# Performance work log

Hardware: AMD Instinct MI355X
Metric: run time of the kernel (lower is better)

The kernel has to match this reference:

```python
import jax, jax.numpy as jnp
import numpy as np
from jax import lax


def _normalizer(x):
    # faithful to: x / norm(x, axis=-1, keepdims=True) + 1e-10
    return x / jnp.linalg.norm(x, axis=-1, keepdims=True) + 1e-10


def setup_inputs() -> dict:
    key = jax.random.key(0)
    k1, k2, k3, k4 = jax.random.split(key, 4)
    Q, D, N, C = 4096, 768, 100000, 1000
    return {
        "feature": jax.random.normal(k1, (Q, D), dtype=jnp.float32),
        "logit": jax.random.normal(k2, (Q, C), dtype=jnp.float32),
        "bank_feas": jax.random.normal(k3, (N, D), dtype=jnp.float32),
        "bank_logits": jax.random.normal(k4, (N, C), dtype=jnp.float32),
        "K": 100,
    }


def reference(feature, logit, bank_feas, bank_logits, K):
    # --- setup(): build bank_guide ---
    bank_confs = jax.nn.logsumexp(bank_logits, axis=-1)          # [N]
    bank_guide = _normalizer(bank_feas) * bank_confs[:, None]    # [N, D]

    # --- forward() ---
    feas_norm = _normalizer(feature)                             # [Q, D]
    energy = jax.nn.logsumexp(logit, axis=-1)                    # [Q]

    # exact kNN inner-product search (faiss IndexFlatIP) = GEMM + top-k
    sims = jnp.einsum("qd,nd->qn", feas_norm, bank_guide)        # [Q, N]
    topk_vals, _ = lax.top_k(sims, K)                            # [Q, K]
    conf = jnp.mean(topk_vals, axis=-1)                          # [Q]

    score = conf * energy
    return -score
```

## Files before the change

kernel.cpp:

```cpp
#include <hip/hip_runtime.h>
#include <hip/hip_bf16.h>

#define QROWS 4096
#define DDIM  768
#define NBANK 100000
#define CDIM  1000
#define KTOP  100
#define NPAD  102400
#define SEGW2 12800
#define LCAP2 4096

typedef float floatx4 __attribute__((ext_vector_type(4)));
typedef short bf16x8 __attribute__((ext_vector_type(8)));

__device__ inline ushort f2bf(float f) {
  uint b = __float_as_uint(f);
  uint r = b + 0x7fffu + ((b >> 16) & 1u);
  return (ushort)(r >> 16);
}
__device__ inline float o16f(ushort u) {
  ushort b = (u & 0x8000) ? (ushort)(u & 0x7fff) : (ushort)~u;
  return __uint_as_float((uint)b << 16);
}

__global__ __launch_bounds__(256) void lse_rows(const float* __restrict__ x,
                                                float* __restrict__ out,
                                                int nrows, int ncols) {
  int row = blockIdx.x * 4 + (threadIdx.x >> 6);
  int lane = threadIdx.x & 63;
  if (row >= nrows) return;
  const float4* rp = (const float4*)(x + (size_t)row * ncols);
  int n4 = ncols >> 2;
  float4 v[4];
  float m = -3.0e38f;
#pragma unroll
  for (int j = 0; j < 4; j++) {
    int idx = lane + j * 64;
    if (idx < n4) {
      v[j] = rp[idx];
      m = fmaxf(m, fmaxf(fmaxf(v[j].x, v[j].y), fmaxf(v[j].z, v[j].w)));
    } else {
      v[j] = make_float4(-3.0e38f, -3.0e38f, -3.0e38f, -3.0e38f);
    }
  }
#pragma unroll
  for (int off = 32; off; off >>= 1) m = fmaxf(m, __shfl_xor(m, off));
  float s = 0.f;
#pragma unroll
  for (int j = 0; j < 4; j++)
    s += __expf(v[j].x - m) + __expf(v[j].y - m) +
         __expf(v[j].z - m) + __expf(v[j].w - m);
#pragma unroll
  for (int off = 32; off; off >>= 1) s += __shfl_xor(s, off);
  if (lane == 0) out[row] = m + __logf(s);
}

__global__ __launch_bounds__(256) void bank_sc(const float* __restrict__ feas,
                                               const float* __restrict__ conf,
                                               ushort* __restrict__ b16) {
  int row = blockIdx.x * 4 + (threadIdx.x >> 6);
  int lane = threadIdx.x & 63;
  if (row >= NPAD) return;
  ushort4* dst = (ushort4*)(b16 + (size_t)row * DDIM);
  if (row >= NBANK) {
#pragma unroll
    for (int j = 0; j < 3; j++) dst[lane + j * 64] = make_ushort4(0, 0, 0, 0);
    return;
  }
  const float4* fp = (const float4*)(feas + (size_t)row * DDIM);
  float4 w[3];
  float ss = 0.f;
#pragma unroll
  for (int j = 0; j < 3; j++) {
    w[j] = fp[lane + j * 64];
    ss += w[j].x * w[j].x + w[j].y * w[j].y + w[j].z * w[j].z + w[j].w * w[j].w;
  }
#pragma unroll
  for (int off = 32; off; off >>= 1) ss += __shfl_xor(ss, off);
  float s = conf[row] / sqrtf(ss);
#pragma unroll
  for (int j = 0; j < 3; j++)
    dst[lane + j * 64] = make_ushort4(f2bf(w[j].x * s), f2bf(w[j].y * s),
                                      f2bf(w[j].z * s), f2bf(w[j].w * s));
}

__global__ __launch_bounds__(256) void feat_norm(const float* __restrict__ x,
                                                 ushort* __restrict__ y) {
  int row = blockIdx.x * 4 + (threadIdx.x >> 6);
  int lane = threadIdx.x & 63;
  if (row >= QROWS) return;
  const float4* rp = (const float4*)(x + (size_t)row * DDIM);
  float4 v[3];
  float ss = 0.f;
#pragma unroll
  for (int j = 0; j < 3; j++) {
    v[j] = rp[lane + j * 64];
    ss += v[j].x * v[j].x + v[j].y * v[j].y + v[j].z * v[j].z + v[j].w * v[j].w;
  }
#pragma unroll
  for (int off = 32; off; off >>= 1) ss += __shfl_xor(ss, off);
  float rn = 1.0f / sqrtf(ss);
  ushort4* dst = (ushort4*)(y + (size_t)row * DDIM);
#pragma unroll
  for (int j = 0; j < 3; j++)
    dst[lane + j * 64] = make_ushort4(f2bf(v[j].x * rn), f2bf(v[j].y * rn),
                                      f2bf(v[j].z * rn), f2bf(v[j].w * rn));
}

#define GBM 256
#define GBN 256
#define GBK 64
#define NT  (DDIM / GBK)
#define GNWG ((QROWS / GBM) * (NPAD / GBN))

__device__ inline void load_lds16(const void* g, void* l) {
  __builtin_amdgcn_global_load_lds(
      (const __attribute__((address_space(1))) void*)g,
      (__attribute__((address_space(3))) void*)l, 16, 0, 0);
}

#define PHASE(BUF, Q, LOADB, STAGE_STMT, VM_STMT)                              \
  {                                                                            \
    const ushort* Ab = lds + (BUF) * 32768;                                    \
    if (LOADB) {                                                               \
      const ushort* Bb = Ab + 16384;                                           \
      _Pragma("unroll") for (int n = 0; n < 4; n++)                            \
        _Pragma("unroll") for (int kk = 0; kk < 2; kk++)                       \
          bfr[n][kk] = *(const bf16x8*)(Bb + (wn * 64 + n * 16 + lr) * 64 +    \
                                        ((kk * 32 + lg * 8) ^ rsw));           \
    }                                                                          \
    bf16x8 af[2][2];                                                           \
    _Pragma("unroll") for (int m = 0; m < 2; m++)                              \
      _Pragma("unroll") for (int kk = 0; kk < 2; kk++)                         \
        af[m][kk] = *(const bf16x8*)(Ab + (wm * 128 + (2 * (Q) + m) * 16 + lr) \
                                     * 64 + ((kk * 32 + lg * 8) ^ rsw));       \
    STAGE_STMT;                                                                \
    __builtin_amdgcn_s_barrier();                                              \
    asm volatile("s_waitcnt lgkmcnt(0)" ::: "memory");                         \
    __builtin_amdgcn_sched_barrier(0);                                         \
    __builtin_amdgcn_s_setprio(1);                                             \
    _Pragma("unroll") for (int m = 0; m < 2; m++)                              \
      _Pragma("unroll") for (int n = 0; n < 4; n++)                            \
        _Pragma("unroll") for (int kk = 0; kk < 2; kk++)                       \
          acc[2 * (Q) + m][n] = __builtin_amdgcn_mfma_f32_16x16x32_bf16(       \
              af[m][kk], bfr[n][kk], acc[2 * (Q) + m][n], 0, 0, 0);            \
    __builtin_amdgcn_s_setprio(0);                                             \
    VM_STMT;                                                                   \
    __builtin_amdgcn_s_barrier();                                              \
  }

__global__ __launch_bounds__(512) void gemm_sims(const ushort* __restrict__ A,
                                                 const ushort* __restrict__ B,
                                                 ushort* __restrict__ C) {
  __shared__ ushort lds[2 * 32768];
  const int tid = threadIdx.x;
  const int lane = tid & 63;
  const int wid = tid >> 6;
  const int wm = wid >> 2, wn = wid & 3;
  const int lr = lane & 15, lg = lane >> 4;

  int flat = blockIdx.x;
  int wgid = (flat & 7) * (GNWG / 8) + (flat >> 3);
  int sup = wgid >> 4, wi = wgid & 15;
  int q_idx = (sup & 3) * 4 + (wi & 3);
  int n_idx = (sup >> 2) * 4 + (wi >> 2);
  const int qBase = q_idx * GBM;
  const int nBase = n_idx * GBN;

  const int rin = lane >> 3;
  const int cswu = ((lane & 7) ^ rin) << 3;
  const int rsw = (lr & 7) << 3;

  auto stageAh = [&](int t, int h) {
    if (t < NT) {
#pragma unroll
      for (int r = 2 * h; r < 2 * h + 2; r++) {
        int G = r * 8 + wid;
        int row = qBase + G * 8 + rin;
        load_lds16(A + (size_t)row * DDIM + t * GBK + cswu,
                   lds + (t & 1) * 32768 + G * 512 + lane * 8);
      }
    }
  };
  auto stageBh = [&](int t, int h) {
    if (t < NT) {
#pragma unroll
      for (int r = 2 * h; r < 2 * h + 2; r++) {
        int G = r * 8 + wid;
        int row = nBase + G * 8 + rin;
        load_lds16(B + (size_t)row * DDIM + t * GBK + cswu,
                   lds + (t & 1) * 32768 + 16384 + G * 512 + lane * 8);
      }
    }
  };

  floatx4 acc[8][4] = {};
  bf16x8 bfr[4][2];

  stageBh(0, 0); stageBh(0, 1);
  stageAh(0, 0); stageAh(0, 1);
  stageBh(1, 0); stageBh(1, 1);
  asm volatile("s_waitcnt vmcnt(4)" ::: "memory");
  __builtin_amdgcn_s_barrier();

#pragma unroll 1
  for (int i = 0; i < NT / 2; i++) {
    const int t0 = 2 * i;
    const bool last = (i == NT / 2 - 1);
    PHASE(0, 0, true,  stageAh(t0 + 1, 0), );
    PHASE(0, 1, false, stageAh(t0 + 1, 1), );
    PHASE(0, 2, false, stageBh(t0 + 2, 0), );
    PHASE(0, 3, false, stageBh(t0 + 2, 1),
          if (last) { asm volatile("s_waitcnt vmcnt(0)" ::: "memory"); }
          else      { asm volatile("s_waitcnt vmcnt(4)" ::: "memory"); });
    PHASE(1, 0, true,  stageAh(t0 + 2, 0), );
    PHASE(1, 1, false, stageAh(t0 + 2, 1), );
    PHASE(1, 2, false, stageBh(t0 + 3, 0), );
    PHASE(1, 3, false, stageBh(t0 + 3, 1),
          if (!last) { asm volatile("s_waitcnt vmcnt(4)" ::: "memory"); });
  }

#pragma unroll
  for (int m = 0; m < 8; m++)
#pragma unroll
    for (int n = 0; n < 4; n++) {
      int q = qBase + wm * 128 + m * 16 + lg * 4;
      int col = nBase + wn * 64 + n * 16 + lr;
      ushort* cp = C + (size_t)q * NPAD + col;
#pragma unroll
      for (int r = 0; r < 4; r++) cp[(size_t)r * NPAD] = f2bf(acc[m][n][r]);
    }
}

__global__ __launch_bounds__(256) void topk_seg(const ushort* __restrict__ sims,
                                                ushort* __restrict__ cand) {
  __shared__ ushort smax[256];
  __shared__ ushort list[LCAP2];
  __shared__ int shC, shM, ipart[4];
  const int t = threadIdx.x;
  const int lane = t & 63;
  const int q = blockIdx.x >> 3, seg = blockIdx.x & 7;
  const ushort* base = sims + (size_t)q * NPAD + seg * SEGW2;

  uint v[25];
#pragma unroll
  for (int i = 0; i < 6; i++) {
    uint4 w = ((const uint4*)base)[i * 256 + t];
    uint ww[4] = {w.x, w.y, w.z, w.w};
#pragma unroll
    for (int e = 0; e < 4; e++) {
      uint u = ww[e];
      uint mm = ((u >> 15) & 0x00010001u) * 0xffffu;
      v[4 * i + e] = (u ^ mm) | (0x80008000u & ~mm);
    }
    if (seg == 7 && (i * 256 + t) >= 1300) {
      v[4 * i] = 0; v[4 * i + 1] = 0; v[4 * i + 2] = 0; v[4 * i + 3] = 0;
    }
  }
  {
    if (seg == 7) {
      v[24] = 0;
    } else {
      uint u = ((const uint*)base)[6144 + t];
      uint mm = ((u >> 15) & 0x00010001u) * 0xffffu;
      v[24] = (u ^ mm) | (0x80008000u & ~mm);
    }
  }
  uint mx = 0;
#pragma unroll
  for (int i = 0; i < 25; i++) {
    uint a = v[i] & 0xffffu, b = v[i] >> 16;
    mx = a > mx ? a : mx;
    mx = b > mx ? b : mx;
  }
  smax[t] = (ushort)mx;
  if (t == 0) shC = 0;
  __syncthreads();

  uint m0 = smax[lane], m1 = smax[lane + 64], m2 = smax[lane + 128], m3 = smax[lane + 192];
  uint lo = 0, hi = 65536;
  while (hi - lo > 1) {
    uint mid = (lo + hi) >> 1;
    int c = __popcll(__ballot(m0 >= mid)) + __popcll(__ballot(m1 >= mid)) +
            __popcll(__ballot(m2 >= mid)) + __popcll(__ballot(m3 >= mid));
    if (c >= KTOP) lo = mid; else hi = mid;
  }
  const uint L = lo;

  const unsigned long long ltm = (1ull << lane) - 1ull;
  int tot = 0;
#pragma unroll
  for (int i = 0; i < 25; i++) {
    tot += __popcll(__ballot((v[i] & 0xffffu) >= L));
    tot += __popcll(__ballot((v[i] >> 16) >= L));
  }
  int wb = 0;
  if (lane == 0) wb = atomicAdd(&shC, tot);
  wb = __shfl(wb, 0);
  int run = wb;
#pragma unroll
  for (int i = 0; i < 25; i++) {
    uint a = v[i] & 0xffffu, b = v[i] >> 16;
    unsigned long long ma = __ballot(a >= L);
    if (a >= L) { int p = run + __popcll(ma & ltm); if (p < LCAP2) list[p] = (ushort)a; }
    run += __popcll(ma);
    unsigned long long mb = __ballot(b >= L);
    if (b >= L) { int p = run + __popcll(mb & ltm); if (p < LCAP2) list[p] = (ushort)b; }
    run += __popcll(mb);
  }
  __syncthreads();
  const int C = shC;

  uint Tkey;
  if (C <= LCAP2) {
    uint lo2 = L, hi2 = 65536;
    while (hi2 - lo2 > 1) {
      uint mid = (lo2 + hi2) >> 1;
      int c = 0;
      for (int j = 0; j < C; j += 64) {
        bool p = (j + lane < C) && ((uint)list[j + lane] >= mid);
        c += __popcll(__ballot(p));
      }
      if (c >= KTOP) lo2 = mid; else hi2 = mid;
    }
    Tkey = lo2;
  } else {
    uint lo2 = L, hi2 = 65536;
    while (hi2 - lo2 > 1) {
      uint mid = (lo2 + hi2) >> 1;
      int c = 0;
#pragma unroll
      for (int i = 0; i < 25; i++) {
        c += ((v[i] & 0xffffu) >= mid) ? 1 : 0;
        c += ((v[i] >> 16) >= mid) ? 1 : 0;
      }
#pragma unroll
      for (int off = 32; off; off >>= 1) c += __shfl_xor(c, off);
      __syncthreads();
      if (lane == 0) ipart[t >> 6] = c;
      __syncthreads();
      c = ipart[0] + ipart[1] + ipart[2] + ipart[3];
      if (c >= KTOP) lo2 = mid; else hi2 = mid;
    }
    Tkey = lo2;
  }

  if (t == 0) shM = 0;
  __syncthreads();
  ushort* dst = cand + (size_t)q * 1024 + seg * 128;
  if (C <= LCAP2) {
    for (int i = t; i < C; i += 256) {
      uint u = list[i];
      if (u > Tkey) { int p = atomicAdd(&shM, 1); dst[p] = (ushort)u; }
    }
  } else {
#pragma unroll
    for (int i = 0; i < 25; i++) {
      uint a = v[i] & 0xffffu, b = v[i] >> 16;
      if (a > Tkey) { int p = atomicAdd(&shM, 1); dst[p] = (ushort)a; }
      if (b > Tkey) { int p = atomicAdd(&shM, 1); dst[p] = (ushort)b; }
    }
  }
  __syncthreads();
  for (int i = shM + t; i < KTOP; i += 256) dst[i] = (ushort)Tkey;
}

__global__ __launch_bounds__(64) void topk_fin(const ushort* __restrict__ cand,
                                               const float* __restrict__ energy,
                                               float* __restrict__ out) {
  const int q = blockIdx.x;
  const int t = threadIdx.x;
  const ushort* row = cand + (size_t)q * 1024;
  ushort kk[16];
#pragma unroll
  for (int s = 0; s < 8; s++) {
    kk[2 * s]     = row[s * 128 + t];
    kk[2 * s + 1] = (t + 64 < KTOP) ? row[s * 128 + 64 + t] : (ushort)0;
  }
  uint lo = 0, hi = 65536;
  while (hi - lo > 1) {
    uint mid = (lo + hi) >> 1;
    int c = 0;
#pragma unroll
    for (int i = 0; i < 16; i++) c += ((uint)kk[i] >= mid) ? 1 : 0;
#pragma unroll
    for (int off = 32; off; off >>= 1) c += __shfl_xor(c, off);
    if (c >= KTOP) lo = mid; else hi = mid;
  }
  const uint T = lo;
  float s = 0.f;
  int m = 0;
#pragma unroll
  for (int i = 0; i < 16; i++) {
    if ((uint)kk[i] > T) { s += o16f(kk[i]); m++; }
  }
#pragma unroll
  for (int off = 32; off; off >>= 1) {
    s += __shfl_xor(s, off);
    m += __shfl_xor(m, off);
  }
  if (t == 0) {
    float total = s + (float)(KTOP - m) * o16f((ushort)T);
    out[q] = -(total * (1.0f / KTOP)) * energy[q];
  }
}

extern "C" void kernel_launch(void* const* d_in, const int* in_sizes, int n_in,
                              void* d_out, int out_size, void* d_ws, size_t ws_size,
                              hipStream_t stream) {
  const float* feature     = (const float*)d_in[0];
  const float* logit       = (const float*)d_in[1];
  const float* bank_feas   = (const float*)d_in[2];
  const float* bank_logits = (const float*)d_in[3];
  float* out = (float*)d_out;

  char* ws = (char*)d_ws;
  size_t off = 0;
  auto take = [&](size_t bytes) -> char* {
    char* p = ws + off;
    off = (off + bytes + 255) & ~(size_t)255;
    return p;
  };
  float*  energy = (float*)take((size_t)QROWS * 4);
  float*  conf   = (float*)take((size_t)NPAD * 4);
  ushort* a16    = (ushort*)take((size_t)QROWS * DDIM * 2);
  ushort* b16    = (ushort*)take((size_t)NPAD * DDIM * 2);
  ushort* sims   = (ushort*)take((size_t)QROWS * NPAD * 2);
  ushort* cand   = (ushort*)take((size_t)QROWS * 1024 * 2);
  if (off > ws_size) return;

  lse_rows <<<dim3((NBANK + 3) / 4), dim3(256), 0, stream>>>(bank_logits, conf, NBANK, CDIM);
  bank_sc  <<<dim3(NPAD / 4), dim3(256), 0, stream>>>(bank_feas, conf, b16);
  lse_rows <<<dim3(QROWS / 4), dim3(256), 0, stream>>>(logit, energy, QROWS, CDIM);
  feat_norm<<<dim3(QROWS / 4), dim3(256), 0, stream>>>(feature, a16);
  gemm_sims<<<dim3(GNWG), dim3(512), 0, stream>>>(a16, b16, sims);
  topk_seg <<<dim3(QROWS * 8), dim3(256), 0, stream>>>(sims, cand);
  topk_fin <<<dim3(QROWS), dim3(64), 0, stream>>>(cand, energy, out);
}
```

Before: 1.122 ms.

## Shrink bank padding and make GEMM workgroups loop over multiple N tiles

Cuts the padded bank width from 102400 to 100352 columns so fewer wasted tiles are computed, and matches the top-k segment width and tail masking to the new size. The GEMM grid becomes 1536 persistent-style workgroups, each keeping its Q tile and streaming 4 or 5 consecutive N tiles through one continuous pipeline. Each workgroup writes out and clears its accumulators after every N tile. LDS fragment addresses are also precomputed outside the loop. The goal is fewer tiles and less pipeline prologue/epilogue overhead, at the cost of an uneven 5-versus-4 tile load across groups and more complex index logic.

```diff
diff --git a/kernel.cpp b/kernel.cpp
--- a/kernel.cpp
+++ b/kernel.cpp
@@ -6,8 +6,8 @@
 #define NBANK 100000
 #define CDIM  1000
 #define KTOP  100
-#define NPAD  102400
-#define SEGW2 12800
+#define NPAD  100352
+#define SEGW2 12544
 #define LCAP2 4096
 
 typedef float floatx4 __attribute__((ext_vector_type(4)));
@@ -17,6 +17,9 @@
   uint b = __float_as_uint(f);
   uint r = b + 0x7fffu + ((b >> 16) & 1u);
   return (ushort)(r >> 16);
+}
+__device__ inline ushort ord16(ushort b) {
+  return (b & 0x8000) ? (ushort)~b : (ushort)(b | 0x8000);
 }
 __device__ inline float o16f(ushort u) {
   ushort b = (u & 0x8000) ? (ushort)(u & 0x7fff) : (ushort)~u;
@@ -110,8 +113,8 @@
 #define GBM 256
 #define GBN 256
 #define GBK 64
-#define NT  (DDIM / GBK)
-#define GNWG ((QROWS / GBM) * (NPAD / GBN))
+#define NT  12
+#define GNWG 1536
 
 __device__ inline void load_lds16(const void* g, void* l) {
   __builtin_amdgcn_global_load_lds(
@@ -121,29 +124,31 @@
 
 #define PHASE(BUF, Q, LOADB, STAGE_STMT, VM_STMT)                              \
   {                                                                            \
-    const ushort* Ab = lds + (BUF) * 32768;                                    \
+    const ushort* Ab = lds + (BUF) * 32768 + aBase;                            \
     if (LOADB) {                                                               \
-      const ushort* Bb = Ab + 16384;                                           \
-      _Pragma("unroll") for (int n = 0; n < 4; n++)                            \
-        _Pragma("unroll") for (int kk = 0; kk < 2; kk++)                       \
-          bfr[n][kk] = *(const bf16x8*)(Bb + (wn * 64 + n * 16 + lr) * 64 +    \
-                                        ((kk * 32 + lg * 8) ^ rsw));           \
+      const ushort* Bb = lds + (BUF) * 32768 + 16384 + bBase;                  \
+      _Pragma("unroll") for (int n = 0; n < 4; n++) {                          \
+        bfr[n][0] = *(const bf16x8*)(Bb + n * 1024 + k0);                      \
+        bfr[n][1] = *(const bf16x8*)(Bb + n * 1024 + k1);                      \
+      }                                                                        \
     }                                                                          \
     bf16x8 af[2][2];                                                           \
-    _Pragma("unroll") for (int m = 0; m < 2; m++)                              \
-      _Pragma("unroll") for (int kk = 0; kk < 2; kk++)                         \
-        af[m][kk] = *(const bf16x8*)(Ab + (wm * 128 + (2 * (Q) + m) * 16 + lr) \
-                                     * 64 + ((kk * 32 + lg * 8) ^ rsw));       \
+    _Pragma("unroll") for (int m = 0; m < 2; m++) {                            \
+      af[m][0] = *(const bf16x8*)(Ab + (2 * (Q) + m) * 1024 + k0);             \
+      af[m][1] = *(const bf16x8*)(Ab + (2 * (Q) + m) * 1024 + k1);             \
+    }                                                                          \
     STAGE_STMT;                                                                \
     __builtin_amdgcn_s_barrier();                                              \
     asm volatile("s_waitcnt lgkmcnt(0)" ::: "memory");                         \
     __builtin_amdgcn_sched_barrier(0);                                         \
     __builtin_amdgcn_s_setprio(1);                                             \
     _Pragma("unroll") for (int m = 0; m < 2; m++)                              \
-      _Pragma("unroll") for (int n = 0; n < 4; n++)                            \
-        _Pragma("unroll") for (int kk = 0; kk < 2; kk++)                       \
-          acc[2 * (Q) + m][n] = __builtin_amdgcn_mfma_f32_16x16x32_bf16(       \
-              af[m][kk], bfr[n][kk], acc[2 * (Q) + m][n], 0, 0, 0);            \
+      _Pragma("unroll") for (int n = 0; n < 4; n++) {                          \
+        acc[2 * (Q) + m][n] = __builtin_amdgcn_mfma_f32_16x16x32_bf16(         \
+            af[m][0], bfr[n][0], acc[2 * (Q) + m][n], 0, 0, 0);                \
+        acc[2 * (Q) + m][n] = __builtin_amdgcn_mfma_f32_16x16x32_bf16(         \
+            af[m][1], bfr[n][1], acc[2 * (Q) + m][n], 0, 0, 0);                \
+      }                                                                        \
     __builtin_amdgcn_s_setprio(0);                                             \
     VM_STMT;                                                                   \
     __builtin_amdgcn_s_barrier();                                              \
@@ -161,75 +166,100 @@
 
   int flat = blockIdx.x;
   int wgid = (flat & 7) * (GNWG / 8) + (flat >> 3);
-  int sup = wgid >> 4, wi = wgid & 15;
-  int q_idx = (sup & 3) * 4 + (wi & 3);
-  int n_idx = (sup >> 2) * 4 + (wi >> 2);
+  int q_idx = wgid & 15;
+  int grp = wgid >> 4;
+  const int nsub = (grp < 8) ? 5 : 4;
+  const int nt0 = (grp < 8) ? 5 * grp : 40 + 4 * (grp - 8);
   const int qBase = q_idx * GBM;
-  const int nBase = n_idx * GBN;
+  const int nStart = nt0 * GBN;
+  const int VTB = NT * nsub;
 
   const int rin = lane >> 3;
   const int cswu = ((lane & 7) ^ rin) << 3;
   const int rsw = (lr & 7) << 3;
 
-  auto stageAh = [&](int t, int h) {
-    if (t < NT) {
-#pragma unroll
-      for (int r = 2 * h; r < 2 * h + 2; r++) {
-        int G = r * 8 + wid;
-        int row = qBase + G * 8 + rin;
-        load_lds16(A + (size_t)row * DDIM + t * GBK + cswu,
-                   lds + (t & 1) * 32768 + G * 512 + lane * 8);
-      }
+  const ushort* aSrc[4];
+  const ushort* bSrc[4];
+  int aDst[4], bDst[4];
+#pragma unroll
+  for (int i = 0; i < 4; i++) {
+    int G = i * 8 + wid;
+    aSrc[i] = A + (size_t)(qBase + G * 8 + rin) * DDIM + cswu;
+    bSrc[i] = B + (size_t)(nStart + G * 8 + rin) * DDIM + cswu;
+    aDst[i] = G * 512 + lane * 8;
+    bDst[i] = 16384 + G * 512 + lane * 8;
+  }
+
+  auto stageA = [&](int vt, int h) {
+    if (vt >= VTB) return;
+    int sub = vt / NT;
+    int kt = vt - sub * NT;
+    int bo = (vt & 1) * 32768;
+#pragma unroll
+    for (int r = 0; r < 2; r++) {
+      int i = 2 * h + r;
+      load_lds16(aSrc[i] + kt * 64, lds + bo + aDst[i]);
     }
   };
-  auto stageBh = [&](int t, int h) {
-    if (t < NT) {
-#pragma unroll
-      for (int r = 2 * h; r < 2 * h + 2; r++) {
-        int G = r * 8 + wid;
-        int row = nBase + G * 8 + rin;
-        load_lds16(B + (size_t)row * DDIM + t * GBK + cswu,
-                   lds + (t & 1) * 32768 + 16384 + G * 512 + lane * 8);
-      }
+  auto stageB = [&](int vt, int h) {
+    if (vt >= VTB) return;
+    int sub = vt / NT;
+    int kt = vt - sub * NT;
+    size_t go = (size_t)sub * (256 * DDIM) + kt * 64;
+    int bo = (vt & 1) * 32768;
+#pragma unroll
+    for (int r = 0; r < 2; r++) {
+      int i = 2 * h + r;
+      load_lds16(bSrc[i] + go, lds + bo + bDst[i]);
     }
   };
 
   floatx4 acc[8][4] = {};
   bf16x8 bfr[4][2];
-
-  stageBh(0, 0); stageBh(0, 1);
-  stageAh(0, 0); stageAh(0, 1);
-  stageBh(1, 0); stageBh(1, 1);
+  const int aBase = (wm * 128 + lr) * 64;
+  const int bBase = (wn * 64 + lr) * 64;
+  const int k0 = (lg * 8) ^ rsw;
+  const int k1 = (32 + lg * 8) ^ rsw;
+
+  stageB(0, 0); stageB(0, 1);
+  stageA(0, 0); stageA(0, 1);
+  stageB(1, 0); stageB(1, 1);
   asm volatile("s_waitcnt vmcnt(4)" ::: "memory");
   __builtin_amdgcn_s_barrier();
 
+  int curN = nStart;
+  const int NP = VTB / 2;
 #pragma unroll 1
-  for (int i = 0; i < NT / 2; i++) {
-    const int t0 = 2 * i;
-    const bool last = (i == NT / 2 - 1);
-    PHASE(0, 0, true,  stageAh(t0 + 1, 0), );
-    PHASE(0, 1, false, stageAh(t0 + 1, 1), );
-    PHASE(0, 2, false, stageBh(t0 + 2, 0), );
-    PHASE(0, 3, false, stageBh(t0 + 2, 1),
-          if (last) { asm volatile("s_waitcnt vmcnt(0)" ::: "memory"); }
-          else      { asm volatile("s_waitcnt vmcnt(4)" ::: "memory"); });
-    PHASE(1, 0, true,  stageAh(t0 + 2, 0), );
-    PHASE(1, 1, false, stageAh(t0 + 2, 1), );
-    PHASE(1, 2, false, stageBh(t0 + 3, 0), );
-    PHASE(1, 3, false, stageBh(t0 + 3, 1),
-          if (!last) { asm volatile("s_waitcnt vmcnt(4)" ::: "memory"); });
-  }
-
-#pragma unroll
-  for (int m = 0; m < 8; m++)
-#pragma unroll
-    for (int n = 0; n < 4; n++) {
-      int q = qBase + wm * 128 + m * 16 + lg * 4;
-      int col = nBase + wn * 64 + n * 16 + lr;
-      ushort* cp = C + (size_t)q * NPAD + col;
-#pragma unroll
-      for (int r = 0; r < 4; r++) cp[(size_t)r * NPAD] = f2bf(acc[m][n][r]);
-    }
+  for (int p = 0; p < NP; p++) {
+    const int t0 = 2 * p;
+    const bool lastp = (p == NP - 1);
+    PHASE(0, 0, true,  stageA(t0 + 1, 0), );
+    PHASE(0, 1, false, stageA(t0 + 1, 1), );
+    PHASE(0, 2, false, stageB(t0 + 2, 0), );
+    PHASE(0, 3, false, stageB(t0 + 2, 1),
+          if (lastp) { asm volatile("s_waitcnt vmcnt(0)" ::: "memory"); }
+          else       { asm volatile("s_waitcnt vmcnt(4)" ::: "memory"); });
+    PHASE(1, 0, true,  stageA(t0 + 2, 0), );
+    PHASE(1, 1, false, stageA(t0 + 2, 1), );
+    PHASE(1, 2, false, stageB(t0 + 3, 0), );
+    PHASE(1, 3, false, stageB(t0 + 3, 1),
+          if (lastp) { asm volatile("s_waitcnt vmcnt(0)" ::: "memory"); }
+          else       { asm volatile("s_waitcnt vmcnt(4)" ::: "memory"); });
+    if ((p % 6) == 5) {
+#pragma unroll
+      for (int m = 0; m < 8; m++)
+#pragma unroll
+        for (int n = 0; n < 4; n++) {
+          int q = qBase + wm * 128 + m * 16 + lg * 4;
+          int col = curN + wn * 64 + n * 16 + lr;
+          ushort* cp = C + (size_t)q * NPAD + col;
+#pragma unroll
+          for (int r = 0; r < 4; r++) cp[(size_t)r * NPAD] = f2bf(acc[m][n][r]);
+          acc[m][n] = (floatx4){0.f, 0.f, 0.f, 0.f};
+        }
+      curN += 256;
+    }
+  }
 }
 
 __global__ __launch_bounds__(256) void topk_seg(const ushort* __restrict__ sims,
@@ -253,19 +283,11 @@
       uint mm = ((u >> 15) & 0x00010001u) * 0xffffu;
       v[4 * i + e] = (u ^ mm) | (0x80008000u & ~mm);
     }
-    if (seg == 7 && (i * 256 + t) >= 1300) {
+    if (seg == 7 && (i * 256 + t) >= 1524) {
       v[4 * i] = 0; v[4 * i + 1] = 0; v[4 * i + 2] = 0; v[4 * i + 3] = 0;
     }
   }
-  {
-    if (seg == 7) {
-      v[24] = 0;
-    } else {
-      uint u = ((const uint*)base)[6144 + t];
-      uint mm = ((u >> 15) & 0x00010001u) * 0xffffu;
-      v[24] = (u ^ mm) | (0x80008000u & ~mm);
-    }
-  }
+  v[24] = (seg == 7) ? 0u : (uint)ord16(base[12288 + t]);
   uint mx = 0;
 #pragma unroll
   for (int i = 0; i < 25; i++) {
@@ -318,8 +340,8 @@
       uint mid = (lo2 + hi2) >> 1;
       int c = 0;
       for (int j = 0; j < C; j += 64) {
-        bool p = (j + lane < C) && ((uint)list[j + lane] >= mid);
-        c += __popcll(__ballot(p));
+        bool pp = (j + lane < C) && ((uint)list[j + lane] >= mid);
+        c += __popcll(__ballot(pp));
       }
       if (c >= KTOP) lo2 = mid; else hi2 = mid;
     }
```

After: 1.191 ms. 1.06x slower.

## Fuse per-tile row maxima into GEMM epilogue and threshold-filter top-k candidates

Applied to the files above, without the earlier changes.

The GEMM epilogue now computes per-row maxima of each 256-wide output tile and writes them to a small rowmax buffer. A new kernel picks, per query, the 100th-largest tile max as a lower bound for the top-k threshold. A filter kernel then streams each sims row once and compacts only values at or above that bound, and the final kernel selects the exact top-100 from this short list, with a full-row fallback if the list overflows. This replaces the multi-pass segmented selection and pads N less (100352), trading some extra epilogue work and atomics for less selection traffic.

```diff
diff --git a/kernel.cpp b/kernel.cpp
--- a/kernel.cpp
+++ b/kernel.cpp
@@ -6,9 +6,9 @@
 #define NBANK 100000
 #define CDIM  1000
 #define KTOP  100
-#define NPAD  102400
-#define SEGW2 12800
-#define LCAP2 4096
+#define NPAD  100352
+#define NTILE 392
+#define CAP   2048
 
 typedef float floatx4 __attribute__((ext_vector_type(4)));
 typedef short bf16x8 __attribute__((ext_vector_type(8)));
@@ -17,6 +17,9 @@
   uint b = __float_as_uint(f);
   uint r = b + 0x7fffu + ((b >> 16) & 1u);
   return (ushort)(r >> 16);
+}
+__device__ inline ushort ord16(ushort b) {
+  return (b & 0x8000) ? (ushort)~b : (ushort)(b | 0x8000);
 }
 __device__ inline float o16f(ushort u) {
   ushort b = (u & 0x8000) ? (ushort)(u & 0x7fff) : (ushort)~u;
@@ -151,7 +154,8 @@
 
 __global__ __launch_bounds__(512) void gemm_sims(const ushort* __restrict__ A,
                                                  const ushort* __restrict__ B,
-                                                 ushort* __restrict__ C) {
+                                                 ushort* __restrict__ C,
+                                                 ushort* __restrict__ rowmax) {
   __shared__ ushort lds[2 * 32768];
   const int tid = threadIdx.x;
   const int lane = tid & 63;
@@ -230,177 +234,194 @@
 #pragma unroll
       for (int r = 0; r < 4; r++) cp[(size_t)r * NPAD] = f2bf(acc[m][n][r]);
     }
-}
-
-__global__ __launch_bounds__(256) void topk_seg(const ushort* __restrict__ sims,
-                                                ushort* __restrict__ cand) {
-  __shared__ ushort smax[256];
-  __shared__ ushort list[LCAP2];
-  __shared__ int shC, shM, ipart[4];
-  const int t = threadIdx.x;
-  const int lane = t & 63;
-  const int q = blockIdx.x >> 3, seg = blockIdx.x & 7;
-  const ushort* base = sims + (size_t)q * NPAD + seg * SEGW2;
-
-  uint v[25];
-#pragma unroll
-  for (int i = 0; i < 6; i++) {
-    uint4 w = ((const uint4*)base)[i * 256 + t];
-    uint ww[4] = {w.x, w.y, w.z, w.w};
-#pragma unroll
-    for (int e = 0; e < 4; e++) {
-      uint u = ww[e];
-      uint mm = ((u >> 15) & 0x00010001u) * 0xffffu;
-      v[4 * i + e] = (u ^ mm) | (0x80008000u & ~mm);
-    }
-    if (seg == 7 && (i * 256 + t) >= 1300) {
-      v[4 * i] = 0; v[4 * i + 1] = 0; v[4 * i + 2] = 0; v[4 * i + 3] = 0;
-    }
-  }
-  {
-    if (seg == 7) {
-      v[24] = 0;
-    } else {
-      uint u = ((const uint*)base)[6144 + t];
-      uint mm = ((u >> 15) & 0x00010001u) * 0xffffu;
-      v[24] = (u ^ mm) | (0x80008000u & ~mm);
-    }
-  }
-  uint mx = 0;
-#pragma unroll
-  for (int i = 0; i < 25; i++) {
-    uint a = v[i] & 0xffffu, b = v[i] >> 16;
-    mx = a > mx ? a : mx;
-    mx = b > mx ? b : mx;
-  }
-  smax[t] = (ushort)mx;
-  if (t == 0) shC = 0;
+
+  ushort* rml = (ushort*)lds;
+#pragma unroll
+  for (int m = 0; m < 8; m++) {
+    uint km[4] = {0u, 0u, 0u, 0u};
+#pragma unroll
+    for (int n = 0; n < 4; n++)
+#pragma unroll
+      for (int r = 0; r < 4; r++) {
+        uint kk = (uint)ord16(f2bf(acc[m][n][r]));
+        km[r] = km[r] > kk ? km[r] : kk;
+      }
+#pragma unroll
+    for (int r = 0; r < 4; r++) {
+      uint kv = km[r];
+#pragma unroll
+      for (int off = 1; off <= 8; off <<= 1) {
+        uint o = __shfl_xor(kv, off);
+        kv = kv > o ? kv : o;
+      }
+      if (lr == 0)
+        rml[(wm * 128 + m * 16 + lg * 4 + r) * 4 + wn] = (ushort)kv;
+    }
+  }
   __syncthreads();
-
-  uint m0 = smax[lane], m1 = smax[lane + 64], m2 = smax[lane + 128], m3 = smax[lane + 192];
-  uint lo = 0, hi = 65536;
-  while (hi - lo > 1) {
-    uint mid = (lo + hi) >> 1;
-    int c = __popcll(__ballot(m0 >= mid)) + __popcll(__ballot(m1 >= mid)) +
-            __popcll(__ballot(m2 >= mid)) + __popcll(__ballot(m3 >= mid));
-    if (c >= KTOP) lo = mid; else hi = mid;
-  }
-  const uint L = lo;
-
-  const unsigned long long ltm = (1ull << lane) - 1ull;
-  int tot = 0;
-#pragma unroll
-  for (int i = 0; i < 25; i++) {
-    tot += __popcll(__ballot((v[i] & 0xffffu) >= L));
-    tot += __popcll(__ballot((v[i] >> 16) >= L));
-  }
-  int wb = 0;
-  if (lane == 0) wb = atomicAdd(&shC, tot);
-  wb = __shfl(wb, 0);
-  int run = wb;
-#pragma unroll
-  for (int i = 0; i < 25; i++) {
-    uint a = v[i] & 0xffffu, b = v[i] >> 16;
-    unsigned long long ma = __ballot(a >= L);
-    if (a >= L) { int p = run + __popcll(ma & ltm); if (p < LCAP2) list[p] = (ushort)a; }
-    run += __popcll(ma);
-    unsigned long long mb = __ballot(b >= L);
-    if (b >= L) { int p = run + __popcll(mb & ltm); if (p < LCAP2) list[p] = (ushort)b; }
-    run += __popcll(mb);
-  }
-  __syncthreads();
-  const int C = shC;
-
-  uint Tkey;
-  if (C <= LCAP2) {
-    uint lo2 = L, hi2 = 65536;
-    while (hi2 - lo2 > 1) {
-      uint mid = (lo2 + hi2) >> 1;
-      int c = 0;
-      for (int j = 0; j < C; j += 64) {
-        bool p = (j + lane < C) && ((uint)list[j + lane] >= mid);
-        c += __popcll(__ballot(p));
-      }
-      if (c >= KTOP) lo2 = mid; else hi2 = mid;
-    }
-    Tkey = lo2;
-  } else {
-    uint lo2 = L, hi2 = 65536;
-    while (hi2 - lo2 > 1) {
-      uint mid = (lo2 + hi2) >> 1;
-      int c = 0;
-#pragma unroll
-      for (int i = 0; i < 25; i++) {
-        c += ((v[i] & 0xffffu) >= mid) ? 1 : 0;
-        c += ((v[i] >> 16) >= mid) ? 1 : 0;
-      }
-#pragma unroll
-      for (int off = 32; off; off >>= 1) c += __shfl_xor(c, off);
-      __syncthreads();
-      if (lane == 0) ipart[t >> 6] = c;
-      __syncthreads();
-      c = ipart[0] + ipart[1] + ipart[2] + ipart[3];
-      if (c >= KTOP) lo2 = mid; else hi2 = mid;
-    }
-    Tkey = lo2;
-  }
-
-  if (t == 0) shM = 0;
-  __syncthreads();
-  ushort* dst = cand + (size_t)q * 1024 + seg * 128;
-  if (C <= LCAP2) {
-    for (int i = t; i < C; i += 256) {
-      uint u = list[i];
-      if (u > Tkey) { int p = atomicAdd(&shM, 1); dst[p] = (ushort)u; }
-    }
-  } else {
-#pragma unroll
-    for (int i = 0; i < 25; i++) {
-      uint a = v[i] & 0xffffu, b = v[i] >> 16;
-      if (a > Tkey) { int p = atomicAdd(&shM, 1); dst[p] = (ushort)a; }
-      if (b > Tkey) { int p = atomicAdd(&shM, 1); dst[p] = (ushort)b; }
-    }
-  }
-  __syncthreads();
-  for (int i = shM + t; i < KTOP; i += 256) dst[i] = (ushort)Tkey;
-}
-
-__global__ __launch_bounds__(64) void topk_fin(const ushort* __restrict__ cand,
-                                               const float* __restrict__ energy,
-                                               float* __restrict__ out) {
-  const int q = blockIdx.x;
-  const int t = threadIdx.x;
-  const ushort* row = cand + (size_t)q * 1024;
-  ushort kk[16];
-#pragma unroll
-  for (int s = 0; s < 8; s++) {
-    kk[2 * s]     = row[s * 128 + t];
-    kk[2 * s + 1] = (t + 64 < KTOP) ? row[s * 128 + 64 + t] : (ushort)0;
+  if (tid < 256) {
+    uint a0 = rml[tid * 4 + 0], a1 = rml[tid * 4 + 1];
+    uint a2 = rml[tid * 4 + 2], a3 = rml[tid * 4 + 3];
+    uint mx = a0 > a1 ? a0 : a1;
+    uint my = a2 > a3 ? a2 : a3;
+    mx = mx > my ? mx : my;
+    rowmax[(size_t)(qBase + tid) * NTILE + n_idx] = (ushort)mx;
+  }
+}
+
+__global__ __launch_bounds__(256) void row_thresh(const ushort* __restrict__ rowmax,
+                                                  ushort* __restrict__ thrv) {
+  int row = blockIdx.x * 4 + (threadIdx.x >> 6);
+  int lane = threadIdx.x & 63;
+  if (row >= QROWS) return;
+  const ushort* rm = rowmax + (size_t)row * NTILE;
+  uint k[7];
+#pragma unroll
+  for (int j = 0; j < 7; j++) {
+    int i = lane + j * 64;
+    k[j] = (i < NTILE) ? (uint)rm[i] : 0u;
   }
   uint lo = 0, hi = 65536;
   while (hi - lo > 1) {
     uint mid = (lo + hi) >> 1;
     int c = 0;
 #pragma unroll
-    for (int i = 0; i < 16; i++) c += ((uint)kk[i] >= mid) ? 1 : 0;
+    for (int j = 0; j < 7; j++) c += (k[j] >= mid) ? 1 : 0;
 #pragma unroll
     for (int off = 32; off; off >>= 1) c += __shfl_xor(c, off);
     if (c >= KTOP) lo = mid; else hi = mid;
   }
-  const uint T = lo;
+  if (lane == 0) thrv[row] = (ushort)lo;
+}
+
+__global__ __launch_bounds__(512) void row_filter(const ushort* __restrict__ sims,
+                                                  const ushort* __restrict__ thrv,
+                                                  ushort* __restrict__ cand,
+                                                  int* __restrict__ cnt) {
+  const int q = blockIdx.x;
+  const int t = threadIdx.x;
+  const int lane = t & 63;
+  const uint Tk = thrv[q];
+  const bool fast = (Tk > 0x8000u);
+  const ushort rawT = (ushort)(Tk & 0x7fffu);
+  const ushort D = (ushort)(0x8000u - (uint)rawT);
+  ushort* dst = cand + (size_t)q * CAP;
+  const uint4* base = (const uint4*)(sims + (size_t)q * NPAD);
+  const unsigned long long ltm = (1ull << lane) - 1ull;
+
+  for (int i = t; i < 12500; i += 512) {
+    uint4 w = base[i];
+    uint u[4] = {w.x, w.y, w.z, w.w};
+    ushort r[8];
+    bool p[8];
+    bool any = false;
+#pragma unroll
+    for (int e = 0; e < 4; e++) {
+      r[2 * e] = (ushort)(u[e] & 0xffffu);
+      r[2 * e + 1] = (ushort)(u[e] >> 16);
+    }
+    if (fast) {
+#pragma unroll
+      for (int j = 0; j < 8; j++) p[j] = (ushort)(r[j] - rawT) < D;
+    } else {
+#pragma unroll
+      for (int j = 0; j < 8; j++) p[j] = (uint)ord16(r[j]) >= Tk;
+    }
+#pragma unroll
+    for (int j = 0; j < 8; j++) any |= p[j];
+    if (__ballot(any)) {
+      unsigned long long mj[8];
+      int tot = 0;
+#pragma unroll
+      for (int j = 0; j < 8; j++) { mj[j] = __ballot(p[j]); tot += __popcll(mj[j]); }
+      int wb = 0;
+      if (lane == 0) wb = atomicAdd(&cnt[q], tot);
+      wb = __shfl(wb, 0);
+      int run = wb;
+#pragma unroll
+      for (int j = 0; j < 8; j++) {
+        if (p[j]) {
+          int pos = run + __popcll(mj[j] & ltm);
+          if (pos < CAP) dst[pos] = r[j];
+        }
+        run += __popcll(mj[j]);
+      }
+    }
+  }
+}
+
+__global__ __launch_bounds__(64) void topk_fin(const ushort* __restrict__ cand,
+                                               const int* __restrict__ cnt,
+                                               const ushort* __restrict__ sims,
+                                               const float* __restrict__ energy,
+                                               float* __restrict__ out) {
+  const int q = blockIdx.x;
+  const int lane = threadIdx.x;
+  const int n = cnt[q];
   float s = 0.f;
   int m = 0;
-#pragma unroll
-  for (int i = 0; i < 16; i++) {
-    if ((uint)kk[i] > T) { s += o16f(kk[i]); m++; }
+  uint Tkey;
+  if (n >= KTOP && n <= CAP) {
+    const ushort* src = cand + (size_t)q * CAP;
+    uint k[32];
+#pragma unroll
+    for (int j = 0; j < 32; j++) {
+      int i = lane + j * 64;
+      k[j] = (i < n) ? (uint)ord16(src[i]) : 0u;
+    }
+    uint lo = 0, hi = 65536;
+    while (hi - lo > 1) {
+      uint mid = (lo + hi) >> 1;
+      int c = 0;
+#pragma unroll
+      for (int j = 0; j < 32; j++) c += (k[j] >= mid) ? 1 : 0;
+#pragma unroll
+      for (int off = 32; off; off >>= 1) c += __shfl_xor(c, off);
+      if (c >= KTOP) lo = mid; else hi = mid;
+    }
+    Tkey = lo;
+#pragma unroll
+    for (int j = 0; j < 32; j++)
+      if (k[j] > Tkey) { s += o16f((ushort)k[j]); m++; }
+  } else {
+    const uint4* base = (const uint4*)(sims + (size_t)q * NPAD);
+    uint lo = 0, hi = 65536;
+    while (hi - lo > 1) {
+      uint mid = (lo + hi) >> 1;
+      int c = 0;
+      for (int i = lane; i < 12500; i += 64) {
+        uint4 w = base[i];
+        uint u[4] = {w.x, w.y, w.z, w.w};
+#pragma unroll
+        for (int e = 0; e < 4; e++) {
+          c += ((uint)ord16((ushort)(u[e] & 0xffffu)) >= mid) ? 1 : 0;
+          c += ((uint)ord16((ushort)(u[e] >> 16)) >= mid) ? 1 : 0;
+        }
+      }
+#pragma unroll
+      for (int off = 32; off; off >>= 1) c += __shfl_xor(c, off);
+      if (c >= KTOP) lo = mid; else hi = mid;
+    }
+    Tkey = lo;
+    for (int i = lane; i < 12500; i += 64) {
+      uint4 w = base[i];
+      uint u[4] = {w.x, w.y, w.z, w.w};
+#pragma unroll
+      for (int e = 0; e < 4; e++) {
+        uint ka = (uint)ord16((ushort)(u[e] & 0xffffu));
+        uint kb = (uint)ord16((ushort)(u[e] >> 16));
+        if (ka > Tkey) { s += o16f((ushort)ka); m++; }
+        if (kb > Tkey) { s += o16f((ushort)kb); m++; }
+      }
+    }
   }
 #pragma unroll
   for (int off = 32; off; off >>= 1) {
     s += __shfl_xor(s, off);
     m += __shfl_xor(m, off);
   }
-  if (t == 0) {
-    float total = s + (float)(KTOP - m) * o16f((ushort)T);
+  if (lane == 0) {
+    float total = s + (float)(KTOP - m) * o16f((ushort)Tkey);
     out[q] = -(total * (1.0f / KTOP)) * energy[q];
   }
 }
@@ -426,14 +447,19 @@
   ushort* a16    = (ushort*)take((size_t)QROWS * DDIM * 2);
   ushort* b16    = (ushort*)take((size_t)NPAD * DDIM * 2);
   ushort* sims   = (ushort*)take((size_t)QROWS * NPAD * 2);
-  ushort* cand   = (ushort*)take((size_t)QROWS * 1024 * 2);
+  ushort* rowmax = (ushort*)take((size_t)QROWS * NTILE * 2);
+  ushort* thrv   = (ushort*)take((size_t)QROWS * 2);
+  int*    cnt    = (int*)take((size_t)QROWS * 4);
+  ushort* cand   = (ushort*)take((size_t)QROWS * CAP * 2);
   if (off > ws_size) return;
 
+  hipMemsetAsync(cnt, 0, (size_t)QROWS * 4, stream);
   lse_rows <<<dim3((NBANK + 3) / 4), dim3(256), 0, stream>>>(bank_logits, conf, NBANK, CDIM);
   bank_sc  <<<dim3(NPAD / 4), dim3(256), 0, stream>>>(bank_feas, conf, b16);
   lse_rows <<<dim3(QROWS / 4), dim3(256), 0, stream>>>(logit, energy, QROWS, CDIM);
   feat_norm<<<dim3(QROWS / 4), dim3(256), 0, stream>>>(feature, a16);
-  gemm_sims<<<dim3(GNWG), dim3(512), 0, stream>>>(a16, b16, sims);
-  topk_seg <<<dim3(QROWS * 8), dim3(256), 0, stream>>>(sims, cand);
-  topk_fin <<<dim3(QROWS), dim3(64), 0, stream>>>(cand, energy, out);
-}
+  gemm_sims<<<dim3(GNWG), dim3(512), 0, stream>>>(a16, b16, sims, rowmax);
+  row_thresh<<<dim3(QROWS / 4), dim3(256), 0, stream>>>(rowmax, thrv);
+  row_filter<<<dim3(QROWS), dim3(512), 0, stream>>>(sims, thrv, cand, cnt);
+  topk_fin <<<dim3(QROWS), dim3(64), 0, stream>>>(cand, cnt, sims, energy, out);
+}
```

Result: slower. 1.173 ms (+4.5%).
